# Performance work log

Measured on AMD Instinct MI355X. Metric: run time of the kernel, lower is better.

The kernel has to match this reference:

```python
import jax, jax.numpy as jnp
import numpy as np

N_NODES = 200000
D = 512
N_EDGES = 12800000


def setup_inputs() -> dict:
    key = jax.random.key(0)
    k1, k2, k3 = jax.random.split(key, 3)
    x = jax.random.normal(k1, (N_NODES, D), dtype=jnp.float32)
    edge_index = jax.random.randint(k2, (2, N_EDGES), 0, N_NODES, dtype=jnp.int64)
    # GCNConv linear weight (glorot-ish scale) and bias
    W = jax.random.normal(k3, (D, 1), dtype=jnp.float32) / np.sqrt(D)
    b = jnp.zeros((1,), dtype=jnp.float32)
    return {"x": x, "edge_index": edge_index, "W": W, "b": b}


def reference(x, edge_index, W, b):
    """one_layer_gcn forward: GCNConv(d, 1) -> ReLU.

    Faithful to PyG GCNConv defaults: add self-loops, symmetric
    deg^{-1/2} normalization, linear transform first (out dim 1),
    scatter-add aggregation into target nodes, bias after aggregation.
    """
    n = x.shape[0]
    loop = jnp.arange(n, dtype=edge_index.dtype)
    src = jnp.concatenate([edge_index[0], loop])  # message sources (x_j)
    dst = jnp.concatenate([edge_index[1], loop])  # aggregation targets

    # degree of target nodes (with self-loops), symmetric normalization
    deg = jax.ops.segment_sum(jnp.ones_like(dst, dtype=x.dtype), dst, num_segments=n)
    dinv = jnp.where(deg > 0, jax.lax.rsqrt(deg), 0.0)
    norm = dinv[src] * dinv[dst]  # [E+N]

    h = x @ W  # [N, 1] -- trivial GEMM, out_channels = 1
    msg = h[src] * norm[:, None]  # gather + weight
    out = jax.ops.segment_sum(msg, dst, num_segments=n)  # scatter-add
    return jax.nn.relu(out + b)
```

## Files before the change

### kernel.cpp

```cpp
#include <hip/hip_runtime.h>


#define GCN_D 512
#define NPB 8192
#define NPB_SHIFT 13
#define MAXNBK 32
#define SPLIT 32
#define CHUNK 8192
#define PT 512
#define P1T 512
#define CPAD 16

__global__ void init_cursor_kernel(int* __restrict__ cursor, int NBK, int CAP) {
    int i = threadIdx.x;
    if (i < NBK) cursor[i * CPAD] = i * CAP;
}

__global__ __launch_bounds__(PT) void place_kernel(const int* __restrict__ src,
                                                   const int* __restrict__ dst,
                                                   int* __restrict__ cursor,
                                                   unsigned int* __restrict__ packed,
                                                   int E, int NBK, int CAP) {
    __shared__ unsigned int staging[CHUNK];
    __shared__ int hist[MAXNBK];
    __shared__ int lstart[MAXNBK];
    __shared__ int lcur[MAXNBK];
    __shared__ int gbase[MAXNBK];

    const int tid = threadIdx.x;
    const int e0 = blockIdx.x * CHUNK;
    const int rem = min(CHUNK, E - e0);
    const int r4 = rem >> 2;

    const int4* d4p = reinterpret_cast<const int4*>(dst + e0);
    const int4* s4p = reinterpret_cast<const int4*>(src + e0);

    if (tid < MAXNBK) hist[tid] = 0;
    __syncthreads();

    int4 dreg[4];
    #pragma unroll
    for (int k = 0; k < 4; ++k) {
        int i4 = tid + k * PT;
        if (i4 < r4) {
            dreg[k] = d4p[i4];
            atomicAdd(&hist[dreg[k].x >> NPB_SHIFT], 1);
            atomicAdd(&hist[dreg[k].y >> NPB_SHIFT], 1);
            atomicAdd(&hist[dreg[k].z >> NPB_SHIFT], 1);
            atomicAdd(&hist[dreg[k].w >> NPB_SHIFT], 1);
        }
    }
    __syncthreads();

    if (tid == 0) {
        int run = 0;
        for (int b = 0; b < NBK; ++b) { lstart[b] = run; lcur[b] = run; run += hist[b]; }
    }
    __syncthreads();
    if (tid < NBK) {
        int c = hist[tid];
        gbase[tid] = c ? atomicAdd(&cursor[tid * CPAD], c) : 0;
    }
    __syncthreads();

    #pragma unroll
    for (int k = 0; k < 4; ++k) {
        int i4 = tid + k * PT;
        if (i4 < r4) {
            int4 s4 = s4p[i4];
            int4 d = dreg[k];
            int b, pos;
            b = d.x >> NPB_SHIFT; pos = atomicAdd(&lcur[b], 1);
            staging[pos] = ((unsigned)s4.x << NPB_SHIFT) | (unsigned)(d.x & (NPB - 1));
            b = d.y >> NPB_SHIFT; pos = atomicAdd(&lcur[b], 1);
            staging[pos] = ((unsigned)s4.y << NPB_SHIFT) | (unsigned)(d.y & (NPB - 1));
            b = d.z >> NPB_SHIFT; pos = atomicAdd(&lcur[b], 1);
            staging[pos] = ((unsigned)s4.z << NPB_SHIFT) | (unsigned)(d.z & (NPB - 1));
            b = d.w >> NPB_SHIFT; pos = atomicAdd(&lcur[b], 1);
            staging[pos] = ((unsigned)s4.w << NPB_SHIFT) | (unsigned)(d.w & (NPB - 1));
        }
    }
    __syncthreads();

    for (int b = 0; b < NBK; ++b) {
        int cnt = hist[b];
        if (!cnt) continue;
        int ls = lstart[b];
        int gb = gbase[b];
        int capend = (b + 1) * CAP;
        for (int p = tid; p < cnt; p += PT) {
            int gp = gb + p;
            if (gp < capend)
                packed[gp] = staging[ls + p];
        }
    }
}

__global__ __launch_bounds__(P1T) void deg_p1_kernel(const unsigned int* __restrict__ packed,
                                                     const int* __restrict__ cursor,
                                                     int* __restrict__ dpart,
                                                     int NBK, int CAP) {
    int b = blockIdx.x / SPLIT;
    int part = blockIdx.x % SPLIT;
    __shared__ int acc[NPB];
    for (int i = threadIdx.x; i < NPB; i += P1T) acc[i] = 0;
    __syncthreads();
    int s0 = b * CAP;
    int s1 = min(cursor[b * CPAD], (b + 1) * CAP);
    int cnt = s1 - s0;
    int n4 = cnt >> 2;
    const uint4* p4 = reinterpret_cast<const uint4*>(packed + s0);
    for (int i = threadIdx.x + part * P1T; i < n4; i += SPLIT * P1T) {
        uint4 p = p4[i];
        atomicAdd(&acc[p.x & (NPB - 1)], 1);
        atomicAdd(&acc[p.y & (NPB - 1)], 1);
        atomicAdd(&acc[p.z & (NPB - 1)], 1);
        atomicAdd(&acc[p.w & (NPB - 1)], 1);
    }
    if (part == 0 && threadIdx.x < (cnt & 3))
        atomicAdd(&acc[packed[s0 + (n4 << 2) + threadIdx.x] & (NPB - 1)], 1);
    __syncthreads();
    int* dp = dpart + (size_t)(b * SPLIT + part) * NPB;
    for (int i = threadIdx.x; i < NPB; i += P1T) dp[i] = acc[i];
}

__global__ void deg_red_kernel(const int* __restrict__ dpart, float* __restrict__ dinv,
                               int n) {
    int v = blockIdx.x * blockDim.x + threadIdx.x;
    if (v < n) {
        int b = v >> NPB_SHIFT;
        int idx = v & (NPB - 1);
        const int* dp = dpart + (size_t)(b * SPLIT) * NPB + idx;
        int s = 0;
        #pragma unroll
        for (int k = 0; k < SPLIT; ++k) s += dp[(size_t)k * NPB];
        dinv[v] = rsqrtf((float)(s + 1));
    }
}

__global__ void gemv_kernel(const float* __restrict__ x, const float* __restrict__ W,
                            const float* __restrict__ dinv, float* __restrict__ hprime,
                            int n) {
    int wave = threadIdx.x >> 6;
    int lane = threadIdx.x & 63;
    int row = blockIdx.x * 4 + wave;
    if (row >= n) return;

    const float4* xr = reinterpret_cast<const float4*>(x + (size_t)row * GCN_D);
    const float4* Wv = reinterpret_cast<const float4*>(W);

    float4 a0 = xr[lane];
    float4 w0 = Wv[lane];
    float4 a1 = xr[lane + 64];
    float4 w1 = Wv[lane + 64];

    float dot = a0.x * w0.x + a0.y * w0.y + a0.z * w0.z + a0.w * w0.w
              + a1.x * w1.x + a1.y * w1.y + a1.z * w1.z + a1.w * w1.w;

    #pragma unroll
    for (int off = 32; off >= 1; off >>= 1)
        dot += __shfl_down(dot, off, 64);

    if (lane == 0) hprime[row] = dot * dinv[row];
}

__global__ __launch_bounds__(P1T) void gather_p1_kernel(const unsigned int* __restrict__ packed,
                                                        const int* __restrict__ cursor,
                                                        const float* __restrict__ hprime,
                                                        float* __restrict__ gpart,
                                                        int NBK, int CAP) {
    int b = blockIdx.x / SPLIT;
    int part = blockIdx.x % SPLIT;
    __shared__ float acc[NPB];
    for (int i = threadIdx.x; i < NPB; i += P1T) acc[i] = 0.f;
    __syncthreads();
    int s0 = b * CAP;
    int s1 = min(cursor[b * CPAD], (b + 1) * CAP);
    int cnt = s1 - s0;
    int n4 = cnt >> 2;
    const uint4* p4 = reinterpret_cast<const uint4*>(packed + s0);
    for (int i = threadIdx.x + part * P1T; i < n4; i += SPLIT * P1T) {
        uint4 p = p4[i];
        atomicAdd(&acc[p.x & (NPB - 1)], hprime[p.x >> NPB_SHIFT]);
        atomicAdd(&acc[p.y & (NPB - 1)], hprime[p.y >> NPB_SHIFT]);
        atomicAdd(&acc[p.z & (NPB - 1)], hprime[p.z >> NPB_SHIFT]);
        atomicAdd(&acc[p.w & (NPB - 1)], hprime[p.w >> NPB_SHIFT]);
    }
    if (part == 0 && threadIdx.x < (cnt & 3)) {
        unsigned p = packed[s0 + (n4 << 2) + threadIdx.x];
        atomicAdd(&acc[p & (NPB - 1)], hprime[p >> NPB_SHIFT]);
    }
    __syncthreads();
    float* gp = gpart + (size_t)(b * SPLIT + part) * NPB;
    for (int i = threadIdx.x; i < NPB; i += P1T) gp[i] = acc[i];
}

__global__ void gather_red_kernel(const float* __restrict__ gpart,
                                  const float* __restrict__ hprime,
                                  const float* __restrict__ dinv,
                                  const float* __restrict__ bias,
                                  float* __restrict__ out, int n) {
    int v = blockIdx.x * blockDim.x + threadIdx.x;
    if (v < n) {
        int b = v >> NPB_SHIFT;
        int idx = v & (NPB - 1);
        const float* gp = gpart + (size_t)(b * SPLIT) * NPB + idx;
        float s = 0.f;
        #pragma unroll
        for (int k = 0; k < SPLIT; ++k) s += gp[(size_t)k * NPB];
        float val = dinv[v] * (s + hprime[v]) + bias[0];
        out[v] = val > 0.f ? val : 0.f;
    }
}

__global__ void deg_atomic_kernel(const int* __restrict__ dst, int* __restrict__ deg, int e4) {
    int i = blockIdx.x * blockDim.x + threadIdx.x;
    if (i < e4) {
        int4 d = reinterpret_cast<const int4*>(dst)[i];
        atomicAdd(&deg[d.x], 1);
        atomicAdd(&deg[d.y], 1);
        atomicAdd(&deg[d.z], 1);
        atomicAdd(&deg[d.w], 1);
    }
}
__global__ void gemv_scaled_fb_kernel(const float* __restrict__ x, const float* __restrict__ W,
                                      const int* __restrict__ deg, float* __restrict__ hprime,
                                      int n) {
    int wave = threadIdx.x >> 6;
    int lane = threadIdx.x & 63;
    int row = blockIdx.x * 4 + wave;
    if (row >= n) return;
    const float4* xr = reinterpret_cast<const float4*>(x + (size_t)row * GCN_D);
    const float4* Wv = reinterpret_cast<const float4*>(W);
    float4 a0 = xr[lane], w0 = Wv[lane];
    float4 a1 = xr[lane + 64], w1 = Wv[lane + 64];
    float dot = a0.x * w0.x + a0.y * w0.y + a0.z * w0.z + a0.w * w0.w
              + a1.x * w1.x + a1.y * w1.y + a1.z * w1.z + a1.w * w1.w;
    #pragma unroll
    for (int off = 32; off >= 1; off >>= 1) dot += __shfl_down(dot, off, 64);
    if (lane == 0) hprime[row] = dot * rsqrtf((float)(deg[row] + 1));
}
__global__ void scatter_kernel(const int* __restrict__ src, const int* __restrict__ dst,
                               const float* __restrict__ hprime, float* __restrict__ acc,
                               int e4) {
    int i = blockIdx.x * blockDim.x + threadIdx.x;
    if (i < e4) {
        int4 s = reinterpret_cast<const int4*>(src)[i];
        int4 d = reinterpret_cast<const int4*>(dst)[i];
        atomicAdd(&acc[d.x], hprime[s.x]);
        atomicAdd(&acc[d.y], hprime[s.y]);
        atomicAdd(&acc[d.z], hprime[s.z]);
        atomicAdd(&acc[d.w], hprime[s.w]);
    }
}
__global__ void final_fb_kernel(const float* __restrict__ hprime, const float* __restrict__ accg,
                                const int* __restrict__ deg, const float* __restrict__ bptr,
                                float* __restrict__ out, int n) {
    int i = blockIdx.x * blockDim.x + threadIdx.x;
    if (i < n) {
        float dinv = rsqrtf((float)(deg[i] + 1));
        float v = dinv * (accg[i] + hprime[i]) + bptr[0];
        out[i] = v > 0.0f ? v : 0.0f;
    }
}

extern "C" void kernel_launch(void* const* d_in, const int* in_sizes, int n_in,
                              void* d_out, int out_size, void* d_ws, size_t ws_size,
                              hipStream_t stream) {
    const float* x    = (const float*)d_in[0];
    const int*   ei   = (const int*)d_in[1];
    const float* W    = (const float*)d_in[2];
    const float* bias = (const float*)d_in[3];
    float* out = (float*)d_out;

    const int n = in_sizes[0] / GCN_D;
    const int E = in_sizes[1] / 2;
    const int e4 = E / 4;

    const int* src = ei;
    const int* dst = ei + E;

    const int NBK = (n + NPB - 1) >> NPB_SHIFT;

    long long lam = ((long long)E * NPB + n - 1) / (n > 0 ? n : 1);
    if (lam < 16) lam = 16;
    long long capll = lam + lam / 8 + 4096;
    int CAP = (int)((capll + 3) & ~3LL);

    auto align64 = [](size_t v) { return (v + 63) & ~(size_t)63; };
    size_t off_dinv   = 0;
    size_t off_hprime = align64(off_dinv   + (size_t)n * 4);
    size_t off_cursor = align64(off_hprime + (size_t)n * 4);
    size_t off_dpart  = align64(off_cursor + (size_t)MAXNBK * CPAD * 4);
    size_t off_gpart  = align64(off_dpart  + (size_t)NBK * SPLIT * NPB * 4);
    size_t off_packed = align64(off_gpart  + (size_t)NBK * SPLIT * NPB * 4);
    size_t needed     = off_packed + (size_t)NBK * CAP * 4;

    char* ws = (char*)d_ws;
    float* dinv   = (float*)(ws + off_dinv);
    float* hprime = (float*)(ws + off_hprime);

    if (NBK <= MAXNBK && n <= (1 << 18) && ws_size >= needed) {
        int* cursor = (int*)(ws + off_cursor);
        int* dpart  = (int*)(ws + off_dpart);
        float* gpart = (float*)(ws + off_gpart);
        unsigned int* packed = (unsigned int*)(ws + off_packed);

        init_cursor_kernel<<<1, 64, 0, stream>>>(cursor, NBK, CAP);
        place_kernel<<<(E + CHUNK - 1) / CHUNK, PT, 0, stream>>>(src, dst, cursor, packed, E, NBK, CAP);
        deg_p1_kernel<<<NBK * SPLIT, P1T, 0, stream>>>(packed, cursor, dpart, NBK, CAP);
        deg_red_kernel<<<(n + 255) / 256, 256, 0, stream>>>(dpart, dinv, n);
        gemv_kernel<<<(n + 3) / 4, 256, 0, stream>>>(x, W, dinv, hprime, n);
        gather_p1_kernel<<<NBK * SPLIT, P1T, 0, stream>>>(packed, cursor, hprime, gpart, NBK, CAP);
        gather_red_kernel<<<(n + 255) / 256, 256, 0, stream>>>(gpart, hprime, dinv, bias, out, n);
    } else {
        int*   deg   = (int*)(ws + off_dinv);
        float* accfb = (float*)(ws + off_cursor);
        hipMemsetAsync(ws, 0, off_cursor + (size_t)n * 4, stream);
        deg_atomic_kernel<<<(e4 + 255) / 256, 256, 0, stream>>>(dst, deg, e4);
        gemv_scaled_fb_kernel<<<(n + 3) / 4, 256, 0, stream>>>(x, W, deg, hprime, n);
        scatter_kernel<<<(e4 + 255) / 256, 256, 0, stream>>>(src, dst, hprime, accfb, e4);
        final_fb_kernel<<<(n + 255) / 256, 256, 0, stream>>>(hprime, accfb, deg, bias, out, n);
    }
}
```

Baseline: 242.7 us.

## Fuse degree histogram and GEMV into one interleaved heterogeneous kernel

Merges the degree-counting pass and the x@W GEMV into a single launch in which some blocks build degree histograms and the remaining blocks compute unscaled dot products, interleaved at a ratio P. The dinv scaling of hprime moves into the degree-reduction kernel, so the GEMV no longer depends on dinv and can overlap the LDS-atomic-bound histogram work with the bandwidth-bound read of x. This removes one launch and lets the two independent stages share the GPU. The cost is an extra read-modify-write of hprime, and the fused kernel always allocates the 32 KB shared histogram, which may reduce occupancy for the GEMV blocks.

Result: slower. 359.9 us (+48.3%).

```diff
diff --git a/kernel.cpp b/kernel.cpp
--- a/kernel.cpp
+++ b/kernel.cpp
@@ -96,36 +96,70 @@
     }
 }
 
-__global__ __launch_bounds__(P1T) void deg_p1_kernel(const unsigned int* __restrict__ packed,
-                                                     const int* __restrict__ cursor,
-                                                     int* __restrict__ dpart,
-                                                     int NBK, int CAP) {
-    int b = blockIdx.x / SPLIT;
-    int part = blockIdx.x % SPLIT;
+__global__ __launch_bounds__(P1T) void fused_dg_kernel(
+        const unsigned int* __restrict__ packed, const int* __restrict__ cursor,
+        int* __restrict__ dpart,
+        const float* __restrict__ x, const float* __restrict__ W,
+        float* __restrict__ hprime,
+        int n, int NBK, int CAP, int DEGB, int P) {
     __shared__ int acc[NPB];
-    for (int i = threadIdx.x; i < NPB; i += P1T) acc[i] = 0;
-    __syncthreads();
-    int s0 = b * CAP;
-    int s1 = min(cursor[b * CPAD], (b + 1) * CAP);
-    int cnt = s1 - s0;
-    int n4 = cnt >> 2;
-    const uint4* p4 = reinterpret_cast<const uint4*>(packed + s0);
-    for (int i = threadIdx.x + part * P1T; i < n4; i += SPLIT * P1T) {
-        uint4 p = p4[i];
-        atomicAdd(&acc[p.x & (NPB - 1)], 1);
-        atomicAdd(&acc[p.y & (NPB - 1)], 1);
-        atomicAdd(&acc[p.z & (NPB - 1)], 1);
-        atomicAdd(&acc[p.w & (NPB - 1)], 1);
-    }
-    if (part == 0 && threadIdx.x < (cnt & 3))
-        atomicAdd(&acc[packed[s0 + (n4 << 2) + threadIdx.x] & (NPB - 1)], 1);
-    __syncthreads();
-    int* dp = dpart + (size_t)(b * SPLIT + part) * NPB;
-    for (int i = threadIdx.x; i < NPB; i += P1T) dp[i] = acc[i];
-}
-
-__global__ void deg_red_kernel(const int* __restrict__ dpart, float* __restrict__ dinv,
-                               int n) {
+
+    const int bid = blockIdx.x;
+    const int tid = threadIdx.x;
+    const bool is_deg = (bid % P == 0) && (bid / P < DEGB);
+
+    if (is_deg) {
+        int db = bid / P;
+        int b = db / SPLIT;
+        int part = db % SPLIT;
+        for (int i = tid; i < NPB; i += P1T) acc[i] = 0;
+        __syncthreads();
+        int s0 = b * CAP;
+        int s1 = min(cursor[b * CPAD], (b + 1) * CAP);
+        int cnt = s1 - s0;
+        int n4 = cnt >> 2;
+        const uint4* p4 = reinterpret_cast<const uint4*>(packed + s0);
+        for (int i = tid + part * P1T; i < n4; i += SPLIT * P1T) {
+            uint4 p = p4[i];
+            atomicAdd(&acc[p.x & (NPB - 1)], 1);
+            atomicAdd(&acc[p.y & (NPB - 1)], 1);
+            atomicAdd(&acc[p.z & (NPB - 1)], 1);
+            atomicAdd(&acc[p.w & (NPB - 1)], 1);
+        }
+        if (part == 0 && tid < (cnt & 3))
+            atomicAdd(&acc[packed[s0 + (n4 << 2) + tid] & (NPB - 1)], 1);
+        __syncthreads();
+        int* dp = dpart + (size_t)(b * SPLIT + part) * NPB;
+        for (int i = tid; i < NPB; i += P1T) dp[i] = acc[i];
+    } else {
+        int gidx = bid - min(bid / P + 1, DEGB);
+        int wave = tid >> 6;
+        int lane = tid & 63;
+        int row = gidx * 8 + wave;
+        if (row >= n) return;
+
+        const float4* xr = reinterpret_cast<const float4*>(x + (size_t)row * GCN_D);
+        const float4* Wv = reinterpret_cast<const float4*>(W);
+
+        float4 a0 = xr[lane];
+        float4 w0 = Wv[lane];
+        float4 a1 = xr[lane + 64];
+        float4 w1 = Wv[lane + 64];
+
+        float dot = a0.x * w0.x + a0.y * w0.y + a0.z * w0.z + a0.w * w0.w
+                  + a1.x * w1.x + a1.y * w1.y + a1.z * w1.z + a1.w * w1.w;
+
+        #pragma unroll
+        for (int off = 32; off >= 1; off >>= 1)
+            dot += __shfl_down(dot, off, 64);
+
+        if (lane == 0) hprime[row] = dot;
+    }
+}
+
+__global__ void deg_red_scale_kernel(const int* __restrict__ dpart,
+                                     float* __restrict__ dinv,
+                                     float* __restrict__ hprime, int n) {
     int v = blockIdx.x * blockDim.x + threadIdx.x;
     if (v < n) {
         int b = v >> NPB_SHIFT;
@@ -134,34 +168,10 @@
         int s = 0;
         #pragma unroll
         for (int k = 0; k < SPLIT; ++k) s += dp[(size_t)k * NPB];
-        dinv[v] = rsqrtf((float)(s + 1));
-    }
-}
-
-__global__ void gemv_kernel(const float* __restrict__ x, const float* __restrict__ W,
-                            const float* __restrict__ dinv, float* __restrict__ hprime,
-                            int n) {
-    int wave = threadIdx.x >> 6;
-    int lane = threadIdx.x & 63;
-    int row = blockIdx.x * 4 + wave;
-    if (row >= n) return;
-
-    const float4* xr = reinterpret_cast<const float4*>(x + (size_t)row * GCN_D);
-    const float4* Wv = reinterpret_cast<const float4*>(W);
-
-    float4 a0 = xr[lane];
-    float4 w0 = Wv[lane];
-    float4 a1 = xr[lane + 64];
-    float4 w1 = Wv[lane + 64];
-
-    float dot = a0.x * w0.x + a0.y * w0.y + a0.z * w0.z + a0.w * w0.w
-              + a1.x * w1.x + a1.y * w1.y + a1.z * w1.z + a1.w * w1.w;
-
-    #pragma unroll
-    for (int off = 32; off >= 1; off >>= 1)
-        dot += __shfl_down(dot, off, 64);
-
-    if (lane == 0) hprime[row] = dot * dinv[row];
+        float dv = rsqrtf((float)(s + 1));
+        dinv[v] = dv;
+        hprime[v] *= dv;
+    }
 }
 
 __global__ __launch_bounds__(P1T) void gather_p1_kernel(const unsigned int* __restrict__ packed,
@@ -192,7 +202,7 @@
     }
     __syncthreads();
     float* gp = gpart + (size_t)(b * SPLIT + part) * NPB;
-    for (int i = threadIdx.x; i < NPB; i += P1T) gp[i] = acc[i];
+    for (int j = threadIdx.x; j < NPB; j += P1T) gp[j] = acc[j];
 }
 
 __global__ void gather_red_kernel(const float* __restrict__ gpart,
@@ -306,11 +316,16 @@
         float* gpart = (float*)(ws + off_gpart);
         unsigned int* packed = (unsigned int*)(ws + off_packed);
 
+        const int DEGB = NBK * SPLIT;
+        const int GEMB = (n + 7) / 8;
+        const int R = DEGB + GEMB;
+        int P = R / DEGB; if (P < 1) P = 1;
+
         init_cursor_kernel<<<1, 64, 0, stream>>>(cursor, NBK, CAP);
         place_kernel<<<(E + CHUNK - 1) / CHUNK, PT, 0, stream>>>(src, dst, cursor, packed, E, NBK, CAP);
-        deg_p1_kernel<<<NBK * SPLIT, P1T, 0, stream>>>(packed, cursor, dpart, NBK, CAP);
-        deg_red_kernel<<<(n + 255) / 256, 256, 0, stream>>>(dpart, dinv, n);
-        gemv_kernel<<<(n + 3) / 4, 256, 0, stream>>>(x, W, dinv, hprime, n);
+        fused_dg_kernel<<<R, P1T, 0, stream>>>(packed, cursor, dpart, x, W, hprime,
+                                               n, NBK, CAP, DEGB, P);
+        deg_red_scale_kernel<<<(n + 255) / 256, 256, 0, stream>>>(dpart, dinv, hprime, n);
         gather_p1_kernel<<<NBK * SPLIT, P1T, 0, stream>>>(packed, cursor, hprime, gpart, NBK, CAP);
         gather_red_kernel<<<(n + 255) / 256, 256, 0, stream>>>(gpart, hprime, dinv, bias, out, n);
     } else {
```
